# Kernel optimization log

Hardware: AMD Instinct MI355X
Metric: run time of the kernel (lower is better)

The kernel has to match this reference:

```python
import jax, jax.numpy as jnp
import numpy as np

EMBED, HEADS, LEVELS, POINTS = 256, 8, 4, 4
HD = EMBED // HEADS
BS, NQ = 2, 16384
SHAPES = [(128, 128), (64, 64), (32, 32), (16, 16)]  # (H, W) per level
NV = sum(h * w for h, w in SHAPES)
EPS = 1e-5


def layernorm(x, g, b):
    mu = jnp.mean(x, -1, keepdims=True)
    var = jnp.mean((x - mu) ** 2, -1, keepdims=True)
    return (x - mu) / jnp.sqrt(var + EPS) * g + b


def bilinear_sample(vl, loc, H, W):
    # vl: (bs, heads, H*W, hd); loc: (bs, nq, heads, P, 2) normalized [0,1]
    # grid_sample semantics: align_corners=False, zero padding
    x = loc[..., 0] * W - 0.5
    y = loc[..., 1] * H - 0.5
    x0 = jnp.floor(x)
    y0 = jnp.floor(y)
    lx, ly = x - x0, y - y0
    x0 = x0.astype(jnp.int32)
    y0 = y0.astype(jnp.int32)
    gather = jax.vmap(jax.vmap(lambda t, i: t[i]))  # over (bs, heads)
    acc = None
    for dx, dy, w in ((0, 0, (1 - lx) * (1 - ly)), (1, 0, lx * (1 - ly)),
                      (0, 1, (1 - lx) * ly), (1, 1, lx * ly)):
        xi, yi = x0 + dx, y0 + dy
        valid = ((xi >= 0) & (xi < W) & (yi >= 0) & (yi < H)).astype(vl.dtype)
        idx = jnp.clip(yi, 0, H - 1) * W + jnp.clip(xi, 0, W - 1)
        idx = idx.transpose(0, 2, 1, 3)           # (bs, heads, nq, P)
        g = gather(vl, idx)                       # (bs, heads, nq, P, hd)
        wv = (w * valid).transpose(0, 2, 1, 3)[..., None]
        acc = g * wv if acc is None else acc + g * wv
    return acc


def forward(lidar_feat, feat_flatten, ref_2d, spatial_shapes, level_start_index,
            q_pose, W_off, b_off, W_attn, b_attn, W_val, b_val, W_out, b_out,
            ln1_g, ln1_b, ffn_w1, ffn_w2, ln2_g, ln2_b):
    identity = lidar_feat                         # (nq, bs, C)
    q = (lidar_feat + q_pose).transpose(1, 0, 2)  # (bs, nq, C)
    bs, nq, C = q.shape
    v = feat_flatten.transpose(1, 0, 2) @ W_val + b_val
    v = v.reshape(bs, -1, HEADS, HD)
    off = (q @ W_off + b_off).reshape(bs, nq, HEADS, LEVELS, POINTS, 2)
    aw = (q @ W_attn + b_attn).reshape(bs, nq, HEADS, LEVELS * POINTS)
    aw = jax.nn.softmax(aw, -1).reshape(bs, nq, HEADS, LEVELS, POINTS)
    ss = np.asarray(spatial_shapes)               # static level shapes
    lsi = np.asarray(level_start_index)
    norm = jnp.asarray(ss[:, ::-1].copy(), q.dtype)  # (L, 2) [W, H]
    loc = ref_2d[:, :, None, :, None, :] + off / norm[None, None, None, :, None, :]
    out = jnp.zeros((bs, nq, HEADS, HD), q.dtype)
    for l in range(LEVELS):
        H, W = int(ss[l, 0]), int(ss[l, 1])
        s = int(lsi[l])
        vl = v[:, s:s + H * W].transpose(0, 2, 1, 3)   # (bs, heads, HW, hd)
        sampled = bilinear_sample(vl, loc[:, :, :, l], H, W)
        out = out + jnp.einsum('bhqpd,bqhp->bqhd', sampled, aw[:, :, :, l, :])
    out = out.reshape(bs, nq, C) @ W_out + b_out
    out = out.transpose(1, 0, 2) + identity       # residual (dropout=eval noop)
    x = layernorm(out, ln1_g, ln1_b)
    x = layernorm(jnp.maximum(x @ ffn_w1, 0.0) @ ffn_w2 + x, ln2_g, ln2_b)
    return x


def setup_inputs():
    key = jax.random.key(0)
    ks = jax.random.split(key, 16)
    starts = np.cumsum([0] + [h * w for h, w in SHAPES])[:-1]
    d = {
        'lidar_feat': jax.random.normal(ks[0], (NQ, BS, EMBED), jnp.float32),
        'feat_flatten': jax.random.normal(ks[1], (NV, BS, EMBED), jnp.float32),
        'ref_2d': jax.random.uniform(ks[2], (BS, NQ, LEVELS, 2), jnp.float32),
        'spatial_shapes': jnp.array(SHAPES, jnp.int32),
        'level_start_index': jnp.array(starts, jnp.int32),
        'q_pose': jax.random.normal(ks[3], (NQ, BS, EMBED), jnp.float32),
        'W_off': 0.02 * jax.random.normal(ks[4], (EMBED, HEADS * LEVELS * POINTS * 2), jnp.float32),
        'b_off': 2.0 * jax.random.normal(ks[5], (HEADS * LEVELS * POINTS * 2,), jnp.float32),
        'W_attn': 0.02 * jax.random.normal(ks[6], (EMBED, HEADS * LEVELS * POINTS), jnp.float32),
        'b_attn': jnp.zeros((HEADS * LEVELS * POINTS,), jnp.float32),
        'W_val': 0.02 * jax.random.normal(ks[7], (EMBED, EMBED), jnp.float32),
        'b_val': jnp.zeros((EMBED,), jnp.float32),
        'W_out': 0.02 * jax.random.normal(ks[8], (EMBED, EMBED), jnp.float32),
        'b_out': jnp.zeros((EMBED,), jnp.float32),
        'ln1_g': jnp.ones((EMBED,), jnp.float32),
        'ln1_b': jnp.zeros((EMBED,), jnp.float32),
        'ffn_w1': 0.02 * jax.random.normal(ks[9], (EMBED, EMBED), jnp.float32),
        'ffn_w2': 0.02 * jax.random.normal(ks[10], (EMBED, EMBED), jnp.float32),
        'ln2_g': jnp.ones((EMBED,), jnp.float32),
        'ln2_b': jnp.zeros((EMBED,), jnp.float32),
    }
    return d


def reference(lidar_feat, feat_flatten, ref_2d, spatial_shapes, level_start_index,
              q_pose, W_off, b_off, W_attn, b_attn, W_val, b_val, W_out, b_out,
              ln1_g, ln1_b, ffn_w1, ffn_w2, ln2_g, ln2_b):
    return forward(lidar_feat, feat_flatten, ref_2d, spatial_shapes,
                   level_start_index, q_pose, W_off, b_off, W_attn, b_attn,
                   W_val, b_val, W_out, b_out, ln1_g, ln1_b, ffn_w1, ffn_w2,
                   ln2_g, ln2_b)
```

## Files before the change

### kernel.cpp

```cpp
#include <hip/hip_runtime.h>
#include <cstdint>

#define EMBED 256
#define HEADS 8
#define LEVELS 4
#define POINTS 4
#define BS 2
#define NQ 16384
#define NV 21760
#define MQ (BS*NQ)
#define MV (BS*NV)

typedef __attribute__((ext_vector_type(8))) short short8;
typedef __attribute__((ext_vector_type(4))) float f32x4;

__device__ __forceinline__ unsigned short f2bf(float f) {
    unsigned int u = __float_as_uint(f);
    u = (u + 0x7FFFu + ((u >> 16) & 1u)) >> 16;
    return (unsigned short)u;
}
__device__ __forceinline__ float bf2f(unsigned short h) {
    return __uint_as_float(((unsigned int)h) << 16);
}
__device__ __forceinline__ void glds16(const unsigned short* g, unsigned short* l) {
    __builtin_amdgcn_global_load_lds((const __attribute__((address_space(1))) void*)g,
                                     (__attribute__((address_space(3))) void*)l, 16, 0, 0);
}

struct WtArgs {
    const float* src[6];
    unsigned short* dst[6];
    int n[6];
};
__global__ __launch_bounds__(256) void prep_wt(WtArgs a)
{
    const int g = blockIdx.y;
    const int N = a.n[g];
    const int e = blockIdx.x * 256 + threadIdx.x;
    if (e >= 256 * N) return;
    const int k = e / N, n = e - k * N;
    a.dst[g][(size_t)n * 256 + k] = f2bf(a.src[g][e]);
}

template<int NCOLS, int STAGEF32, int LNF, int RELUF>
__global__ __launch_bounds__(512) void gemm_big(
    const unsigned short* __restrict__ A,
    const float* __restrict__ Af, const float* __restrict__ A2f, int inner,
    const unsigned short* __restrict__ Bt,
    const float* __restrict__ bias0, const float* __restrict__ bias1,
    const float* __restrict__ res,
    const float* __restrict__ lng, const float* __restrict__ lnb,
    float* __restrict__ outf, unsigned short* __restrict__ outh)
{
    constexpr int FN = NCOLS / 64;
    __shared__ unsigned short As[128 * 32];
    __shared__ unsigned short Bs[NCOLS * 32];
    __shared__ float2 sdLN[LNF ? 128 : 1][4];

    const int t = threadIdx.x, l = t & 63, w = t >> 6;
    const int wm = w >> 2, wn = w & 3;
    const int frow = l & 15, fgrp = l >> 4;
    const size_t brow = (size_t)blockIdx.x * 128;

    const int fslot = fgrp ^ ((frow & 3) ^ ((frow >> 2) & 3));
    const int srow = l >> 2;
    const int sswz = (l & 3) ^ ((srow & 3) ^ ((srow >> 2) & 3));
    const unsigned short* gB0 = Bt + ((size_t)(w * 16 + srow)) * 256 + sswz * 8;

    const unsigned short* gA = nullptr;
    const float* srcA = nullptr; const float* srcA2 = nullptr;
    int arow_s = 0, aslot_s = 0, aswz_s = 0;
    if constexpr (STAGEF32) {
        arow_s = t >> 2; aslot_s = t & 3;
        const int grow = (int)brow + arow_s;
        const int bidx = grow / inner, nn = grow - bidx * inner;
        srcA = Af + (size_t)(nn * BS + bidx) * 256;
        if (A2f) srcA2 = A2f + (size_t)(nn * BS + bidx) * 256;
        aswz_s = aslot_s ^ ((arow_s & 3) ^ ((arow_s >> 2) & 3));
    } else {
        gA = A + (brow + (size_t)(w * 16 + srow)) * 256 + sswz * 8;
    }

    f32x4 acc[4][FN];
#pragma unroll
    for (int i = 0; i < 4; ++i)
#pragma unroll
        for (int j = 0; j < FN; ++j) acc[i][j] = f32x4{0.f, 0.f, 0.f, 0.f};

    float4 pA0, pA1, pC0, pC1;
    if constexpr (STAGEF32) {
        pA0 = *(const float4*)(srcA + aslot_s * 8);
        pA1 = *(const float4*)(srcA + aslot_s * 8 + 4);
        if (srcA2) { pC0 = *(const float4*)(srcA2 + aslot_s * 8);
                     pC1 = *(const float4*)(srcA2 + aslot_s * 8 + 4); }
    }

    for (int k0 = 0; k0 < 256; k0 += 32) {
        glds16(gB0 + k0,         (unsigned short*)&Bs[w * 512]);
        glds16(gB0 + 32768 + k0, (unsigned short*)&Bs[(w + 8) * 512]);
        if constexpr (NCOLS == 384)
            glds16(gB0 + 65536 + k0, (unsigned short*)&Bs[(w + 16) * 512]);

        if constexpr (STAGEF32) {
            float c[8] = {pA0.x, pA0.y, pA0.z, pA0.w, pA1.x, pA1.y, pA1.z, pA1.w};
            if (srcA2) {
                c[0] += pC0.x; c[1] += pC0.y; c[2] += pC0.z; c[3] += pC0.w;
                c[4] += pC1.x; c[5] += pC1.y; c[6] += pC1.z; c[7] += pC1.w;
            }
            short8 pk;
#pragma unroll
            for (int i = 0; i < 8; ++i) pk[i] = (short)f2bf(c[i]);
            *reinterpret_cast<short8*>(&As[arow_s * 32 + aswz_s * 8]) = pk;
            if (k0 + 32 < 256) {
                pA0 = *(const float4*)(srcA + k0 + 32 + aslot_s * 8);
                pA1 = *(const float4*)(srcA + k0 + 32 + aslot_s * 8 + 4);
                if (srcA2) { pC0 = *(const float4*)(srcA2 + k0 + 32 + aslot_s * 8);
                             pC1 = *(const float4*)(srcA2 + k0 + 32 + aslot_s * 8 + 4); }
            }
        } else {
            glds16(gA + k0, (unsigned short*)&As[w * 512]);
        }
        __syncthreads();

        short8 af[4]; short8 bq[FN];
#pragma unroll
        for (int fm = 0; fm < 4; ++fm)
            af[fm] = *reinterpret_cast<const short8*>(&As[(wm * 64 + fm * 16 + frow) * 32 + fslot * 8]);
#pragma unroll
        for (int fn = 0; fn < FN; ++fn)
            bq[fn] = *reinterpret_cast<const short8*>(&Bs[(wn * (NCOLS / 4) + fn * 16 + frow) * 32 + fslot * 8]);
#pragma unroll
        for (int fm = 0; fm < 4; ++fm)
#pragma unroll
            for (int fn = 0; fn < FN; ++fn)
                acc[fm][fn] = __builtin_amdgcn_mfma_f32_16x16x32_bf16(af[fm], bq[fn], acc[fm][fn], 0, 0, 0);
        __syncthreads();
    }

    int cols[FN]; float bi[FN];
#pragma unroll
    for (int fn = 0; fn < FN; ++fn) {
        const int col = wn * (NCOLS / 4) + fn * 16 + frow;
        cols[fn] = col;
        float b = 0.f;
        if (bias0) {
            if (NCOLS == 384) b = (col < 256) ? bias0[col] : bias1[col - 256];
            else              b = bias0[col];
        }
        bi[fn] = b;
    }
#pragma unroll
    for (int fm = 0; fm < 4; ++fm)
#pragma unroll
        for (int j = 0; j < 4; ++j) {
            const size_t row = brow + wm * 64 + fm * 16 + fgrp * 4 + j;
#pragma unroll
            for (int fn = 0; fn < FN; ++fn) {
                float x = acc[fm][fn][j] + bi[fn];
                if (res)   x += res[row * NCOLS + cols[fn]];
                if (RELUF) x = fmaxf(x, 0.f);
                acc[fm][fn][j] = x;
            }
        }

    if constexpr (LNF) {
#pragma unroll
        for (int fm = 0; fm < 4; ++fm)
#pragma unroll
            for (int j = 0; j < 4; ++j) {
                float s1 = 0.f, s2 = 0.f;
#pragma unroll
                for (int fn = 0; fn < FN; ++fn) { const float x = acc[fm][fn][j]; s1 += x; s2 += x * x; }
#pragma unroll
                for (int o = 1; o < 16; o <<= 1) { s1 += __shfl_xor(s1, o); s2 += __shfl_xor(s2, o); }
                if (frow == 0)
                    sdLN[wm * 64 + fm * 16 + fgrp * 4 + j][wn] = make_float2(s1, s2);
            }
        __syncthreads();
        float gv[FN], bv[FN];
#pragma unroll
        for (int fn = 0; fn < FN; ++fn) { gv[fn] = lng[cols[fn]]; bv[fn] = lnb[cols[fn]]; }
#pragma unroll
        for (int fm = 0; fm < 4; ++fm)
#pragma unroll
            for (int j = 0; j < 4; ++j) {
                const int rl = wm * 64 + fm * 16 + fgrp * 4 + j;
                const float2 p0 = sdLN[rl][0], p1 = sdLN[rl][1], p2 = sdLN[rl][2], p3 = sdLN[rl][3];
                const float s1 = p0.x + p1.x + p2.x + p3.x;
                const float s2 = p0.y + p1.y + p2.y + p3.y;
                const float mu = s1 * (1.f / 256.f);
                const float var = s2 * (1.f / 256.f) - mu * mu;
                const float rstd = rsqrtf(var + 1e-5f);
                const size_t row = brow + rl;
#pragma unroll
                for (int fn = 0; fn < FN; ++fn) {
                    const float y = (acc[fm][fn][j] - mu) * rstd * gv[fn] + bv[fn];
                    if (outf) outf[row * NCOLS + cols[fn]] = y;
                    if (outh) outh[row * NCOLS + cols[fn]] = f2bf(y);
                }
            }
    } else {
#pragma unroll
        for (int fm = 0; fm < 4; ++fm)
#pragma unroll
            for (int j = 0; j < 4; ++j) {
                const size_t row = brow + wm * 64 + fm * 16 + fgrp * 4 + j;
#pragma unroll
                for (int fn = 0; fn < FN; ++fn) {
                    const float x = acc[fm][fn][j];
                    if (outf) outf[row * NCOLS + cols[fn]] = x;
                    if (outh) outh[row * NCOLS + cols[fn]] = f2bf(x);
                }
            }
    }
}

__global__ __launch_bounds__(512) void ffn_fused(
    const unsigned short* __restrict__ X,
    const unsigned short* __restrict__ W1t, const unsigned short* __restrict__ W2t,
    const float* __restrict__ lng, const float* __restrict__ lnb,
    float* __restrict__ outf)
{
    __shared__ unsigned short As[64 * 32];
    __shared__ unsigned short Bs[256 * 32];
    __shared__ unsigned short Hs[64 * 256];
    __shared__ float2 sdLN[64][4];

    const int t = threadIdx.x, l = t & 63, w = t >> 6;
    const int wm = w >> 2, wn = w & 3;
    const int frow = l & 15, fgrp = l >> 4;
    const size_t brow = (size_t)blockIdx.x * 64;

    const int fslot = fgrp ^ ((frow & 3) ^ ((frow >> 2) & 3));
    const int srow = l >> 2;
    const int sswz = (l & 3) ^ ((srow & 3) ^ ((srow >> 2) & 3));

    const unsigned short* gX  = X + (brow + (size_t)((w & 3) * 16 + srow)) * 256 + sswz * 8;
    const unsigned short* gW1 = W1t + ((size_t)(w * 16 + srow)) * 256 + sswz * 8;
    const unsigned short* gW2 = W2t + ((size_t)(w * 16 + srow)) * 256 + sswz * 8;

    f32x4 acc[2][4];

#pragma unroll
    for (int i = 0; i < 2; ++i)
#pragma unroll
        for (int j = 0; j < 4; ++j) acc[i][j] = f32x4{0.f, 0.f, 0.f, 0.f};

    for (int k0 = 0; k0 < 256; k0 += 32) {
        glds16(gW1 + k0,         (unsigned short*)&Bs[w * 512]);
        glds16(gW1 + 32768 + k0, (unsigned short*)&Bs[(w + 8) * 512]);
        if (w < 4) glds16(gX + k0, (unsigned short*)&As[w * 512]);
        __syncthreads();

        short8 af[2], bq[4];
#pragma unroll
        for (int fm = 0; fm < 2; ++fm)
            af[fm] = *reinterpret_cast<const short8*>(&As[(wm * 32 + fm * 16 + frow) * 32 + fslot * 8]);
#pragma unroll
        for (int fn = 0; fn < 4; ++fn)
            bq[fn] = *reinterpret_cast<const short8*>(&Bs[(wn * 64 + fn * 16 + frow) * 32 + fslot * 8]);
#pragma unroll
        for (int fm = 0; fm < 2; ++fm)
#pragma unroll
            for (int fn = 0; fn < 4; ++fn)
                acc[fm][fn] = __builtin_amdgcn_mfma_f32_16x16x32_bf16(af[fm], bq[fn], acc[fm][fn], 0, 0, 0);
        __syncthreads();
    }

#pragma unroll
    for (int fm = 0; fm < 2; ++fm)
#pragma unroll
        for (int fn = 0; fn < 4; ++fn) {
            const int col = wn * 64 + fn * 16 + frow;
#pragma unroll
            for (int j = 0; j < 4; ++j) {
                const int row = wm * 32 + fm * 16 + fgrp * 4 + j;
                const int ss = (col >> 3) ^ (row & 7);
                Hs[row * 256 + ss * 8 + (col & 7)] = f2bf(fmaxf(acc[fm][fn][j], 0.f));
            }
        }
    __syncthreads();

#pragma unroll
    for (int i = 0; i < 2; ++i)
#pragma unroll
        for (int j = 0; j < 4; ++j) acc[i][j] = f32x4{0.f, 0.f, 0.f, 0.f};

    for (int k0 = 0; k0 < 256; k0 += 32) {
        glds16(gW2 + k0,         (unsigned short*)&Bs[w * 512]);
        glds16(gW2 + 32768 + k0, (unsigned short*)&Bs[(w + 8) * 512]);
        __syncthreads();

        short8 af[2], bq[4];
#pragma unroll
        for (int fm = 0; fm < 2; ++fm) {
            const int row = wm * 32 + fm * 16 + frow;
            const int ksg = (k0 >> 3) + fgrp;
            const int ss = ksg ^ (row & 7);
            af[fm] = *reinterpret_cast<const short8*>(&Hs[row * 256 + ss * 8]);
        }
#pragma unroll
        for (int fn = 0; fn < 4; ++fn)
            bq[fn] = *reinterpret_cast<const short8*>(&Bs[(wn * 64 + fn * 16 + frow) * 32 + fslot * 8]);
#pragma unroll
        for (int fm = 0; fm < 2; ++fm)
#pragma unroll
            for (int fn = 0; fn < 4; ++fn)
                acc[fm][fn] = __builtin_amdgcn_mfma_f32_16x16x32_bf16(af[fm], bq[fn], acc[fm][fn], 0, 0, 0);
        __syncthreads();
    }

#pragma unroll
    for (int fm = 0; fm < 2; ++fm)
#pragma unroll
        for (int fn = 0; fn < 4; ++fn) {
            const int col = wn * 64 + fn * 16 + frow;
#pragma unroll
            for (int j = 0; j < 4; ++j) {
                const size_t row = brow + wm * 32 + fm * 16 + fgrp * 4 + j;
                acc[fm][fn][j] += bf2f(X[row * 256 + col]);
            }
        }
#pragma unroll
    for (int fm = 0; fm < 2; ++fm)
#pragma unroll
        for (int j = 0; j < 4; ++j) {
            float s1 = 0.f, s2 = 0.f;
#pragma unroll
            for (int fn = 0; fn < 4; ++fn) { const float x = acc[fm][fn][j]; s1 += x; s2 += x * x; }
#pragma unroll
            for (int o = 1; o < 16; o <<= 1) { s1 += __shfl_xor(s1, o); s2 += __shfl_xor(s2, o); }
            if (frow == 0)
                sdLN[wm * 32 + fm * 16 + fgrp * 4 + j][wn] = make_float2(s1, s2);
        }
    __syncthreads();
#pragma unroll
    for (int fm = 0; fm < 2; ++fm)
#pragma unroll
        for (int j = 0; j < 4; ++j) {
            const int rl = wm * 32 + fm * 16 + fgrp * 4 + j;
            const float2 p0 = sdLN[rl][0], p1 = sdLN[rl][1], p2 = sdLN[rl][2], p3 = sdLN[rl][3];
            const float s1 = p0.x + p1.x + p2.x + p3.x;
            const float s2 = p0.y + p1.y + p2.y + p3.y;
            const float mu = s1 * (1.f / 256.f);
            const float var = s2 * (1.f / 256.f) - mu * mu;
            const float rstd = rsqrtf(var + 1e-5f);
            const size_t row = brow + rl;
#pragma unroll
            for (int fn = 0; fn < 4; ++fn) {
                const int col = wn * 64 + fn * 16 + frow;
                outf[row * 256 + col] = (acc[fm][fn][j] - mu) * rstd * lng[col] + lnb[col];
            }
        }
}

#define LDDESC(dst, base)                         \
    _Pragma("unroll")                             \
    for (int j = 0; j < 16; ++j) dst[j] = dp[(base) + j];
#define LDRAW(dst, dsc)                           \
    _Pragma("unroll")                             \
    for (int j = 0; j < 16; ++j) dst[j] = *(const uint2*)(vd + dsc[j].y);
#define FMA16(dsc, raw)                           \
    _Pragma("unroll")                             \
    for (int j = 0; j < 16; ++j) {                \
        const float wgt = __uint_as_float(dsc[j].x);            \
        a0 += wgt * __uint_as_float(raw[j].x << 16);            \
        a1 += wgt * __uint_as_float(raw[j].x & 0xFFFF0000u);    \
        a2 += wgt * __uint_as_float(raw[j].y << 16);            \
        a3 += wgt * __uint_as_float(raw[j].y & 0xFFFF0000u);    \
    }

__global__ __launch_bounds__(256) void sampler_k(
    const unsigned short* __restrict__ oa,
    const float* __restrict__ ref2d,
    const unsigned short* __restrict__ v,
    unsigned short* __restrict__ outh)
{
    const int q0 = blockIdx.x * 4;
    const int t = threadIdx.x;

    __shared__ float s_off[4][256];
    __shared__ float s_aw[4][128];
    __shared__ float s_ref[4][8];
    __shared__ uint2 s_d[4][8][65];

    {
        const int tq = t >> 6, c = (t & 63) * 4;
        const ushort4 u = *(const ushort4*)(oa + (size_t)(q0 + tq) * 384 + c);
        s_off[tq][c + 0] = bf2f(u.x); s_off[tq][c + 1] = bf2f(u.y);
        s_off[tq][c + 2] = bf2f(u.z); s_off[tq][c + 3] = bf2f(u.w);
    }
    if (t < 128) {
        const int tq = t >> 5, c = (t & 31) * 4;
        const ushort4 u = *(const ushort4*)(oa + (size_t)(q0 + tq) * 384 + 256 + c);
        s_aw[tq][c + 0] = bf2f(u.x); s_aw[tq][c + 1] = bf2f(u.y);
        s_aw[tq][c + 2] = bf2f(u.z); s_aw[tq][c + 3] = bf2f(u.w);
    }
    if (t < 32) {
        const int tq = t >> 3;
        s_ref[tq][t & 7] = ref2d[(size_t)(q0 + tq) * 8 + (t & 7)];
    }
    __syncthreads();

    if (t < 32) {
        const int tq = t >> 3, h = t & 7;
        float* a = s_aw[tq] + h * 16;
        float m = -1e30f;
#pragma unroll
        for (int i = 0; i < 16; ++i) m = fmaxf(m, a[i]);
        float e[16], s = 0.f;
#pragma unroll
        for (int i = 0; i < 16; ++i) { e[i] = __expf(a[i] - m); s += e[i]; }
        const float inv = 1.f / s;
#pragma unroll
        for (int i = 0; i < 16; ++i) a[i] = e[i] * inv;
    }
    __syncthreads();

#pragma unroll
    for (int it = 0; it < 2; ++it) {
        const int item = t + it * 256;
        const int tq = item >> 7, hlp = item & 127;
        const int h = hlp >> 4, lp = hlp & 15, li = lp >> 2;
        const int Wl[4]  = {128, 64, 32, 16};
        const int S0l[4] = {0, 16384, 20480, 21504};
        const int Wi = Wl[li]; const float Wf = (float)Wi;
        const int b = (q0 + tq) >> 14;
        const float x = (s_ref[tq][li * 2 + 0] + s_off[tq][hlp * 2 + 0] / Wf) * Wf - 0.5f;
        const float y = (s_ref[tq][li * 2 + 1] + s_off[tq][hlp * 2 + 1] / Wf) * Wf - 0.5f;
        const float x0f = floorf(x), y0f = floorf(y);
        const float lx = x - x0f, ly = y - y0f;
        const int x0 = (int)x0f, y0 = (int)y0f;
        const float a = s_aw[tq][hlp];
        const float cw[4] = {(1.f - lx) * (1.f - ly) * a, lx * (1.f - ly) * a,
                             (1.f - lx) * ly * a,          lx * ly * a};
        const int base = b * NV + S0l[li];
#pragma unroll
        for (int c = 0; c < 4; ++c) {
            const int xi = x0 + (c & 1), yi = y0 + (c >> 1);
            const bool val = (xi >= 0) & (xi < Wi) & (yi >= 0) & (yi < Wi);
            const int xc = min(max(xi, 0), Wi - 1), yc = min(max(yi, 0), Wi - 1);
            const unsigned int ofs = (unsigned int)(base + yc * Wi + xc) * 256u + h * 32;
            s_d[tq][h][lp * 4 + c] = make_uint2(__float_as_uint(val ? cw[c] : 0.f), ofs);
        }
    }
    __syncthreads();

    const int tq = t >> 6, l = t & 63, h = l >> 3, dq = l & 7;
    const int rb = q0 + tq, b = rb >> 14, qi = rb & (NQ - 1);
    const unsigned short* vd = v + dq * 4;
    const uint2* dp = &s_d[tq][h][0];
    float a0 = 0.f, a1 = 0.f, a2 = 0.f, a3 = 0.f;

    uint2 dA[16], dB[16], rA[16], rB[16];
    LDDESC(dA, 0)
    LDRAW(rA, dA)
    LDDESC(dB, 16)
    LDRAW(rB, dB)
    FMA16(dA, rA)
    LDDESC(dA, 32)
    LDRAW(rA, dA)
    FMA16(dB, rB)
    LDDESC(dB, 48)
    LDRAW(rB, dB)
    FMA16(dA, rA)
    FMA16(dB, rB)

    ushort4 o; o.x = f2bf(a0); o.y = f2bf(a1); o.z = f2bf(a2); o.w = f2bf(a3);
    *(ushort4*)(outh + (size_t)(qi * BS + b) * 256 + h * 32 + dq * 4) = o;
}

extern "C" void kernel_launch(void* const* d_in, const int* in_sizes, int n_in,
                              void* d_out, int out_size, void* d_ws, size_t ws_size,
                              hipStream_t stream)
{
    const float* lidar  = (const float*)d_in[0];
    const float* feat   = (const float*)d_in[1];
    const float* ref2d  = (const float*)d_in[2];
    const float* q_pose = (const float*)d_in[5];
    const float* W_off  = (const float*)d_in[6];
    const float* b_off  = (const float*)d_in[7];
    const float* W_attn = (const float*)d_in[8];
    const float* b_attn = (const float*)d_in[9];
    const float* W_val  = (const float*)d_in[10];
    const float* b_val  = (const float*)d_in[11];
    const float* W_out  = (const float*)d_in[12];
    const float* b_out  = (const float*)d_in[13];
    const float* ln1_g  = (const float*)d_in[14];
    const float* ln1_b  = (const float*)d_in[15];
    const float* ffn_w1 = (const float*)d_in[16];
    const float* ffn_w2 = (const float*)d_in[17];
    const float* ln2_g  = (const float*)d_in[18];
    const float* ln2_b  = (const float*)d_in[19];

    float* out = (float*)d_out;
    char*  ws  = (char*)d_ws;

    unsigned short* vb   = (unsigned short*)(ws + 0);
    unsigned short* oa   = (unsigned short*)(ws + 22282240);
    unsigned short* smp  = (unsigned short*)(ws + 47448064);
    unsigned short* xln  = (unsigned short*)(ws + 64225280);
    unsigned short* wt   = (unsigned short*)(ws + 81002496);
    unsigned short* wt_val = wt;
    unsigned short* wt_oa  = wt + 65536;
    unsigned short* wt_out = wt + 163840;
    unsigned short* wt_f1  = wt + 229376;
    unsigned short* wt_f2  = wt + 294912;

    WtArgs wa;
    wa.src[0] = W_val;  wa.dst[0] = wt_val;          wa.n[0] = 256;
    wa.src[1] = W_off;  wa.dst[1] = wt_oa;           wa.n[1] = 256;
    wa.src[2] = W_attn; wa.dst[2] = wt_oa + 65536;   wa.n[2] = 128;
    wa.src[3] = W_out;  wa.dst[3] = wt_out;          wa.n[3] = 256;
    wa.src[4] = ffn_w1; wa.dst[4] = wt_f1;           wa.n[4] = 256;
    wa.src[5] = ffn_w2; wa.dst[5] = wt_f2;           wa.n[5] = 256;
    prep_wt<<<dim3(384, 6), dim3(256), 0, stream>>>(wa);

    gemm_big<256, 1, 0, 0><<<dim3(MV / 128), dim3(512), 0, stream>>>(
        nullptr, feat, nullptr, NV, wt_val, b_val, nullptr,
        nullptr, nullptr, nullptr, nullptr, vb);

    gemm_big<384, 1, 0, 0><<<dim3(MQ / 128), dim3(512), 0, stream>>>(
        nullptr, lidar, q_pose, NQ, wt_oa, b_off, b_attn,
        nullptr, nullptr, nullptr, nullptr, oa);

    sampler_k<<<dim3(MQ / 4), dim3(256), 0, stream>>>(oa, ref2d, vb, smp);

    gemm_big<256, 0, 1, 0><<<dim3(MQ / 128), dim3(512), 0, stream>>>(
        smp, nullptr, nullptr, 0, wt_out, b_out, nullptr,
        lidar, ln1_g, ln1_b, nullptr, xln);

    ffn_fused<<<dim3(MQ / 64), dim3(512), 0, stream>>>(
        xln, wt_f1, wt_f2, ln2_g, ln2_b, out);
}
```

Before: 204.5 us.

## Fuse value/offset GEMMs, sort queries spatially, and fuse out-proj with FFN

```diff
diff --git a/kernel.cpp b/kernel.cpp
--- a/kernel.cpp
+++ b/kernel.cpp
@@ -10,6 +10,9 @@
 #define NV 21760
 #define MQ (BS*NQ)
 #define MV (BS*NV)
+#define VAL_BLK 340
+#define OA_BLK  256
+#define BKT_BLK 64
 
 typedef __attribute__((ext_vector_type(8))) short short8;
 typedef __attribute__((ext_vector_type(4))) float f32x4;
@@ -32,54 +35,43 @@
     unsigned short* dst[6];
     int n[6];
 };
-__global__ __launch_bounds__(256) void prep_wt(WtArgs a)
-{
+__global__ __launch_bounds__(256) void prep_wt(WtArgs a, int* __restrict__ hist)
+{
+    const int t = threadIdx.x;
+    if (blockIdx.x == 0 && blockIdx.y == 0) { hist[t] = 0; hist[t + 256] = 0; }
     const int g = blockIdx.y;
     const int N = a.n[g];
-    const int e = blockIdx.x * 256 + threadIdx.x;
+    const int e = blockIdx.x * 256 + t;
     if (e >= 256 * N) return;
     const int k = e / N, n = e - k * N;
     a.dst[g][(size_t)n * 256 + k] = f2bf(a.src[g][e]);
 }
 
-template<int NCOLS, int STAGEF32, int LNF, int RELUF>
-__global__ __launch_bounds__(512) void gemm_big(
-    const unsigned short* __restrict__ A,
+template<int NCOLS>
+__device__ __forceinline__ void gemm_core(
+    unsigned short* As, unsigned short* Bs, int bx,
     const float* __restrict__ Af, const float* __restrict__ A2f, int inner,
     const unsigned short* __restrict__ Bt,
     const float* __restrict__ bias0, const float* __restrict__ bias1,
-    const float* __restrict__ res,
-    const float* __restrict__ lng, const float* __restrict__ lnb,
-    float* __restrict__ outf, unsigned short* __restrict__ outh)
+    unsigned short* __restrict__ outh)
 {
     constexpr int FN = NCOLS / 64;
-    __shared__ unsigned short As[128 * 32];
-    __shared__ unsigned short Bs[NCOLS * 32];
-    __shared__ float2 sdLN[LNF ? 128 : 1][4];
-
     const int t = threadIdx.x, l = t & 63, w = t >> 6;
     const int wm = w >> 2, wn = w & 3;
     const int frow = l & 15, fgrp = l >> 4;
-    const size_t brow = (size_t)blockIdx.x * 128;
+    const size_t brow = (size_t)bx * 128;
 
     const int fslot = fgrp ^ ((frow & 3) ^ ((frow >> 2) & 3));
     const int srow = l >> 2;
     const int sswz = (l & 3) ^ ((srow & 3) ^ ((srow >> 2) & 3));
     const unsigned short* gB0 = Bt + ((size_t)(w * 16 + srow)) * 256 + sswz * 8;
 
-    const unsigned short* gA = nullptr;
-    const float* srcA = nullptr; const float* srcA2 = nullptr;
-    int arow_s = 0, aslot_s = 0, aswz_s = 0;
-    if constexpr (STAGEF32) {
-        arow_s = t >> 2; aslot_s = t & 3;
-        const int grow = (int)brow + arow_s;
-        const int bidx = grow / inner, nn = grow - bidx * inner;
-        srcA = Af + (size_t)(nn * BS + bidx) * 256;
-        if (A2f) srcA2 = A2f + (size_t)(nn * BS + bidx) * 256;
-        aswz_s = aslot_s ^ ((arow_s & 3) ^ ((arow_s >> 2) & 3));
-    } else {
-        gA = A + (brow + (size_t)(w * 16 + srow)) * 256 + sswz * 8;
-    }
+    const int arow_s = t >> 2, aslot_s = t & 3;
+    const int grow = (int)brow + arow_s;
+    const int bidx = grow / inner, nn = grow - bidx * inner;
+    const float* srcA = Af + (size_t)(nn * BS + bidx) * 256;
+    const float* srcA2 = A2f ? A2f + (size_t)(nn * BS + bidx) * 256 : nullptr;
+    const int aswz_s = aslot_s ^ ((arow_s & 3) ^ ((arow_s >> 2) & 3));
 
     f32x4 acc[4][FN];
 #pragma unroll
@@ -87,38 +79,32 @@
 #pragma unroll
         for (int j = 0; j < FN; ++j) acc[i][j] = f32x4{0.f, 0.f, 0.f, 0.f};
 
-    float4 pA0, pA1, pC0, pC1;
-    if constexpr (STAGEF32) {
-        pA0 = *(const float4*)(srcA + aslot_s * 8);
-        pA1 = *(const float4*)(srcA + aslot_s * 8 + 4);
-        if (srcA2) { pC0 = *(const float4*)(srcA2 + aslot_s * 8);
-                     pC1 = *(const float4*)(srcA2 + aslot_s * 8 + 4); }
-    }
+    float4 pA0 = *(const float4*)(srcA + aslot_s * 8);
+    float4 pA1 = *(const float4*)(srcA + aslot_s * 8 + 4);
+    float4 pC0, pC1;
+    if (srcA2) { pC0 = *(const float4*)(srcA2 + aslot_s * 8);
+                 pC1 = *(const float4*)(srcA2 + aslot_s * 8 + 4); }
 
     for (int k0 = 0; k0 < 256; k0 += 32) {
-        glds16(gB0 + k0,         (unsigned short*)&Bs[w * 512]);
-        glds16(gB0 + 32768 + k0, (unsigned short*)&Bs[(w + 8) * 512]);
+        glds16(gB0 + k0,         &Bs[w * 512]);
+        glds16(gB0 + 32768 + k0, &Bs[(w + 8) * 512]);
         if constexpr (NCOLS == 384)
-            glds16(gB0 + 65536 + k0, (unsigned short*)&Bs[(w + 16) * 512]);
-
-        if constexpr (STAGEF32) {
-            float c[8] = {pA0.x, pA0.y, pA0.z, pA0.w, pA1.x, pA1.y, pA1.z, pA1.w};
-            if (srcA2) {
-                c[0] += pC0.x; c[1] += pC0.y; c[2] += pC0.z; c[3] += pC0.w;
-                c[4] += pC1.x; c[5] += pC1.y; c[6] += pC1.z; c[7] += pC1.w;
-            }
-            short8 pk;
-#pragma unroll
-            for (int i = 0; i < 8; ++i) pk[i] = (short)f2bf(c[i]);
-            *reinterpret_cast<short8*>(&As[arow_s * 32 + aswz_s * 8]) = pk;
-            if (k0 + 32 < 256) {
-                pA0 = *(const float4*)(srcA + k0 + 32 + aslot_s * 8);
-                pA1 = *(const float4*)(srcA + k0 + 32 + aslot_s * 8 + 4);
-                if (srcA2) { pC0 = *(const float4*)(srcA2 + k0 + 32 + aslot_s * 8);
-                             pC1 = *(const float4*)(srcA2 + k0 + 32 + aslot_s * 8 + 4); }
-            }
-        } else {
-            glds16(gA + k0, (unsigned short*)&As[w * 512]);
+            glds16(gB0 + 65536 + k0, &Bs[(w + 16) * 512]);
+
+        float c[8] = {pA0.x, pA0.y, pA0.z, pA0.w, pA1.x, pA1.y, pA1.z, pA1.w};
+        if (srcA2) {
+            c[0] += pC0.x; c[1] += pC0.y; c[2] += pC0.z; c[3] += pC0.w;
+            c[4] += pC1.x; c[5] += pC1.y; c[6] += pC1.z; c[7] += pC1.w;
+        }
+        short8 pk;
+#pragma unroll
+        for (int i = 0; i < 8; ++i) pk[i] = (short)f2bf(c[i]);
+        *reinterpret_cast<short8*>(&As[arow_s * 32 + aswz_s * 8]) = pk;
+        if (k0 + 32 < 256) {
+            pA0 = *(const float4*)(srcA + k0 + 32 + aslot_s * 8);
+            pA1 = *(const float4*)(srcA + k0 + 32 + aslot_s * 8 + 4);
+            if (srcA2) { pC0 = *(const float4*)(srcA2 + k0 + 32 + aslot_s * 8);
+                         pC1 = *(const float4*)(srcA2 + k0 + 32 + aslot_s * 8 + 4); }
         }
         __syncthreads();
 
@@ -137,93 +123,166 @@
         __syncthreads();
     }
 
-    int cols[FN]; float bi[FN];
 #pragma unroll
     for (int fn = 0; fn < FN; ++fn) {
         const int col = wn * (NCOLS / 4) + fn * 16 + frow;
-        cols[fn] = col;
         float b = 0.f;
-        if (bias0) {
-            if (NCOLS == 384) b = (col < 256) ? bias0[col] : bias1[col - 256];
-            else              b = bias0[col];
-        }
-        bi[fn] = b;
-    }
-#pragma unroll
-    for (int fm = 0; fm < 4; ++fm)
-#pragma unroll
-        for (int j = 0; j < 4; ++j) {
-            const size_t row = brow + wm * 64 + fm * 16 + fgrp * 4 + j;
-#pragma unroll
-            for (int fn = 0; fn < FN; ++fn) {
-                float x = acc[fm][fn][j] + bi[fn];
-                if (res)   x += res[row * NCOLS + cols[fn]];
-                if (RELUF) x = fmaxf(x, 0.f);
-                acc[fm][fn][j] = x;
-            }
-        }
-
-    if constexpr (LNF) {
-#pragma unroll
-        for (int fm = 0; fm < 4; ++fm)
-#pragma unroll
-            for (int j = 0; j < 4; ++j) {
-                float s1 = 0.f, s2 = 0.f;
-#pragma unroll
-                for (int fn = 0; fn < FN; ++fn) { const float x = acc[fm][fn][j]; s1 += x; s2 += x * x; }
-#pragma unroll
-                for (int o = 1; o < 16; o <<= 1) { s1 += __shfl_xor(s1, o); s2 += __shfl_xor(s2, o); }
-                if (frow == 0)
-                    sdLN[wm * 64 + fm * 16 + fgrp * 4 + j][wn] = make_float2(s1, s2);
-            }
-        __syncthreads();
-        float gv[FN], bv[FN];
-#pragma unroll
-        for (int fn = 0; fn < FN; ++fn) { gv[fn] = lng[cols[fn]]; bv[fn] = lnb[cols[fn]]; }
-#pragma unroll
-        for (int fm = 0; fm < 4; ++fm)
-#pragma unroll
-            for (int j = 0; j < 4; ++j) {
-                const int rl = wm * 64 + fm * 16 + fgrp * 4 + j;
-                const float2 p0 = sdLN[rl][0], p1 = sdLN[rl][1], p2 = sdLN[rl][2], p3 = sdLN[rl][3];
-                const float s1 = p0.x + p1.x + p2.x + p3.x;
-                const float s2 = p0.y + p1.y + p2.y + p3.y;
-                const float mu = s1 * (1.f / 256.f);
-                const float var = s2 * (1.f / 256.f) - mu * mu;
-                const float rstd = rsqrtf(var + 1e-5f);
-                const size_t row = brow + rl;
-#pragma unroll
-                for (int fn = 0; fn < FN; ++fn) {
-                    const float y = (acc[fm][fn][j] - mu) * rstd * gv[fn] + bv[fn];
-                    if (outf) outf[row * NCOLS + cols[fn]] = y;
-                    if (outh) outh[row * NCOLS + cols[fn]] = f2bf(y);
-                }
-            }
-    } else {
+        if (NCOLS == 384) b = (col < 256) ? bias0[col] : bias1[col - 256];
+        else              b = bias0[col];
 #pragma unroll
         for (int fm = 0; fm < 4; ++fm)
 #pragma unroll
             for (int j = 0; j < 4; ++j) {
                 const size_t row = brow + wm * 64 + fm * 16 + fgrp * 4 + j;
-#pragma unroll
-                for (int fn = 0; fn < FN; ++fn) {
-                    const float x = acc[fm][fn][j];
-                    if (outf) outf[row * NCOLS + cols[fn]] = x;
-                    if (outh) outh[row * NCOLS + cols[fn]] = f2bf(x);
-                }
+                outh[row * NCOLS + col] = f2bf(acc[fm][fn][j] + b);
             }
     }
 }
 
-__global__ __launch_bounds__(512) void ffn_fused(
-    const unsigned short* __restrict__ X,
-    const unsigned short* __restrict__ W1t, const unsigned short* __restrict__ W2t,
-    const float* __restrict__ lng, const float* __restrict__ lnb,
+__global__ __launch_bounds__(512) void valoa_k(
+    const float* __restrict__ feat, const float* __restrict__ lidar,
+    const float* __restrict__ q_pose, const float* __restrict__ ref2d,
+    const unsigned short* __restrict__ wt_val, const unsigned short* __restrict__ wt_oa,
+    const float* __restrict__ b_val, const float* __restrict__ b_off,
+    const float* __restrict__ b_attn,
+    unsigned short* __restrict__ vb, unsigned short* __restrict__ oa,
+    int* __restrict__ bkt, int* __restrict__ hist)
+{
+    __shared__ unsigned short As[128 * 32];
+    __shared__ unsigned short Bs[384 * 32];
+    const int bx = blockIdx.x;
+    if (bx < VAL_BLK) {
+        gemm_core<256>(As, Bs, bx, feat, nullptr, NV, wt_val, b_val, nullptr, vb);
+    } else if (bx < VAL_BLK + OA_BLK) {
+        gemm_core<384>(As, Bs, bx - VAL_BLK, lidar, q_pose, NQ, wt_oa, b_off, b_attn, oa);
+    } else {
+        const int rb = (bx - VAL_BLK - OA_BLK) * 512 + threadIdx.x;
+        const float x = ref2d[(size_t)rb * 8 + 0];
+        const float y = ref2d[(size_t)rb * 8 + 1];
+        const int qx = min(15, max(0, (int)(x * 16.f)));
+        const int qy = min(15, max(0, (int)(y * 16.f)));
+        const int bv = (rb >> 14) * 256 + qy * 16 + qx;
+        bkt[rb] = bv;
+        atomicAdd(&hist[bv], 1);
+    }
+}
+
+__global__ __launch_bounds__(512) void scan_scatter_k(
+    const int* __restrict__ hist, const int* __restrict__ bkt, int* __restrict__ perm)
+{
+    __shared__ int s[512];
+    __shared__ int cur[512];
+    const int t = threadIdx.x;
+    const int v = hist[t];
+    s[t] = v;
+    __syncthreads();
+    int acc = v;
+#pragma unroll
+    for (int o = 1; o < 512; o <<= 1) {
+        const int add = (t >= o) ? s[t - o] : 0;
+        __syncthreads();
+        acc += add;
+        s[t] = acc;
+        __syncthreads();
+    }
+    cur[t] = acc - v;
+    __syncthreads();
+#pragma unroll 4
+    for (int i = 0; i < 64; ++i) {
+        const int rb = i * 512 + t;
+        const int pos = atomicAdd(&cur[bkt[rb]], 1);
+        perm[pos] = rb;
+    }
+}
+
+__global__ __launch_bounds__(256) void sampler_k(
+    const unsigned short* __restrict__ oa,
+    const float* __restrict__ ref2d,
+    const unsigned short* __restrict__ v,
+    const int* __restrict__ perm,
+    unsigned short* __restrict__ outh)
+{
+    const int bid = blockIdx.x;
+    const int sbid = (bid & 7) * (MQ / 4 / 8) + (bid >> 3);
+    const int q0 = sbid * 4;
+    const int t = threadIdx.x;
+
+    __shared__ uint2 s_d[4][8][4][17];
+
+#pragma unroll
+    for (int it = 0; it < 2; ++it) {
+        const int item = t + it * 256;
+        const int tq = item >> 7, hlp = item & 127;
+        const int h = hlp >> 4, lp = hlp & 15, li = lp >> 2;
+        const int rb = perm[q0 + tq];
+        const int b = rb >> 14;
+
+        const float2 refv = *(const float2*)(ref2d + (size_t)rb * 8 + li * 2);
+        const ushort2 offu = *(const ushort2*)(oa + (size_t)rb * 384 + hlp * 2);
+        const float ax = bf2f(oa[(size_t)rb * 384 + 256 + hlp]);
+
+        float m = ax;
+#pragma unroll
+        for (int o = 1; o < 16; o <<= 1) m = fmaxf(m, __shfl_xor(m, o));
+        const float e = __expf(ax - m);
+        float sden = e;
+#pragma unroll
+        for (int o = 1; o < 16; o <<= 1) sden += __shfl_xor(sden, o);
+        const float a = e / sden;
+
+        const int Wl[4]  = {128, 64, 32, 16};
+        const int S0l[4] = {0, 16384, 20480, 21504};
+        const int Wi = Wl[li]; const float Wf = (float)Wi;
+        const float x = (refv.x + bf2f(offu.x) / Wf) * Wf - 0.5f;
+        const float y = (refv.y + bf2f(offu.y) / Wf) * Wf - 0.5f;
+        const float x0f = floorf(x), y0f = floorf(y);
+        const float lx = x - x0f, ly = y - y0f;
+        const int x0 = (int)x0f, y0 = (int)y0f;
+        const float cw[4] = {(1.f - lx) * (1.f - ly) * a, lx * (1.f - ly) * a,
+                             (1.f - lx) * ly * a,          lx * ly * a};
+        const int base = b * NV + S0l[li];
+#pragma unroll
+        for (int c = 0; c < 4; ++c) {
+            const int xi = x0 + (c & 1), yi = y0 + (c >> 1);
+            const bool val = (xi >= 0) & (xi < Wi) & (yi >= 0) & (yi < Wi);
+            const int xc = min(max(xi, 0), Wi - 1), yc = min(max(yi, 0), Wi - 1);
+            const unsigned int ofs = (unsigned int)(base + yc * Wi + xc) * 256u + h * 32;
+            s_d[tq][h][c][lp] = make_uint2(__float_as_uint(val ? cw[c] : 0.f), ofs);
+        }
+    }
+    __syncthreads();
+
+    const int tq = t >> 6, l = t & 63, h = l >> 3, dq = l & 7;
+    const int rb = perm[q0 + tq], b = rb >> 14, qi = rb & (NQ - 1);
+    const unsigned short* vd = v + dq * 4;
+    float a0 = 0.f, a1 = 0.f, a2 = 0.f, a3 = 0.f;
+#pragma unroll
+    for (int c = 0; c < 4; ++c) {
+#pragma unroll
+        for (int i = 0; i < 16; ++i) {
+            const uint2 dd = s_d[tq][h][c][i];
+            const uint2 raw = *(const uint2*)(vd + dd.y);
+            const float wgt = __uint_as_float(dd.x);
+            a0 += wgt * __uint_as_float(raw.x << 16);
+            a1 += wgt * __uint_as_float(raw.x & 0xFFFF0000u);
+            a2 += wgt * __uint_as_float(raw.y << 16);
+            a3 += wgt * __uint_as_float(raw.y & 0xFFFF0000u);
+        }
+    }
+    ushort4 o; o.x = f2bf(a0); o.y = f2bf(a1); o.z = f2bf(a2); o.w = f2bf(a3);
+    *(ushort4*)(outh + (size_t)(qi * BS + b) * 256 + h * 32 + dq * 4) = o;
+}
+
+__global__ __launch_bounds__(512) void mega_k(
+    const unsigned short* __restrict__ smp, const float* __restrict__ lidar,
+    const unsigned short* __restrict__ Wo, const unsigned short* __restrict__ W1,
+    const unsigned short* __restrict__ W2, const float* __restrict__ b_out,
+    const float* __restrict__ ln1g, const float* __restrict__ ln1b,
+    const float* __restrict__ ln2g, const float* __restrict__ ln2b,
     float* __restrict__ outf)
 {
-    __shared__ unsigned short As[64 * 32];
+    __shared__ unsigned short XH[64 * 256];
     __shared__ unsigned short Bs[256 * 32];
-    __shared__ unsigned short Hs[64 * 256];
     __shared__ float2 sdLN[64][4];
 
     const int t = threadIdx.x, l = t & 63, w = t >> 6;
@@ -235,11 +294,13 @@
     const int srow = l >> 2;
     const int sswz = (l & 3) ^ ((srow & 3) ^ ((srow >> 2) & 3));
 
-    const unsigned short* gX  = X + (brow + (size_t)((w & 3) * 16 + srow)) * 256 + sswz * 8;
-    const unsigned short* gW1 = W1t + ((size_t)(w * 16 + srow)) * 256 + sswz * 8;
-    const unsigned short* gW2 = W2t + ((size_t)(w * 16 + srow)) * 256 + sswz * 8;
+    const unsigned short* gA  = smp + (brow + (size_t)((w & 3) * 16 + srow)) * 256 + sswz * 8;
+    const unsigned short* gWo = Wo + ((size_t)(w * 16 + srow)) * 256 + sswz * 8;
+    const unsigned short* gW1 = W1 + ((size_t)(w * 16 + srow)) * 256 + sswz * 8;
+    const unsigned short* gW2 = W2 + ((size_t)(w * 16 + srow)) * 256 + sswz * 8;
 
     f32x4 acc[2][4];
+    f32x4 xres[2][4];
 
 #pragma unroll
     for (int i = 0; i < 2; ++i)
@@ -247,15 +308,14 @@
         for (int j = 0; j < 4; ++j) acc[i][j] = f32x4{0.f, 0.f, 0.f, 0.f};
 
     for (int k0 = 0; k0 < 256; k0 += 32) {
-        glds16(gW1 + k0,         (unsigned short*)&Bs[w * 512]);
-        glds16(gW1 + 32768 + k0, (unsigned short*)&Bs[(w + 8) * 512]);
-        if (w < 4) glds16(gX + k0, (unsigned short*)&As[w * 512]);
-        __syncthreads();
-
+        glds16(gWo + k0,         &Bs[w * 512]);
+        glds16(gWo + 32768 + k0, &Bs[(w + 8) * 512]);
+        if (w < 4) glds16(gA + k0, &XH[w * 512]);
+        __syncthreads();
         short8 af[2], bq[4];
 #pragma unroll
         for (int fm = 0; fm < 2; ++fm)
-            af[fm] = *reinterpret_cast<const short8*>(&As[(wm * 32 + fm * 16 + frow) * 32 + fslot * 8]);
+            af[fm] = *reinterpret_cast<const short8*>(&XH[(wm * 32 + fm * 16 + frow) * 32 + fslot * 8]);
 #pragma unroll
         for (int fn = 0; fn < 4; ++fn)
             bq[fn] = *reinterpret_cast<const short8*>(&Bs[(wn * 64 + fn * 16 + frow) * 32 + fslot * 8]);
@@ -272,13 +332,45 @@
 #pragma unroll
         for (int fn = 0; fn < 4; ++fn) {
             const int col = wn * 64 + fn * 16 + frow;
+            const float bv = b_out[col];
 #pragma unroll
             for (int j = 0; j < 4; ++j) {
-                const int row = wm * 32 + fm * 16 + fgrp * 4 + j;
-                const int ss = (col >> 3) ^ (row & 7);
-                Hs[row * 256 + ss * 8 + (col & 7)] = f2bf(fmaxf(acc[fm][fn][j], 0.f));
+                const size_t row = brow + wm * 32 + fm * 16 + fgrp * 4 + j;
+                acc[fm][fn][j] += bv + lidar[row * 256 + col];
             }
         }
+#pragma unroll
+    for (int fm = 0; fm < 2; ++fm)
+#pragma unroll
+        for (int j = 0; j < 4; ++j) {
+            float s1 = 0.f, s2 = 0.f;
+#pragma unroll
+            for (int fn = 0; fn < 4; ++fn) { const float x = acc[fm][fn][j]; s1 += x; s2 += x * x; }
+#pragma unroll
+            for (int o = 1; o < 16; o <<= 1) { s1 += __shfl_xor(s1, o); s2 += __shfl_xor(s2, o); }
+            if (frow == 0) sdLN[wm * 32 + fm * 16 + fgrp * 4 + j][wn] = make_float2(s1, s2);
+        }
+    __syncthreads();
+#pragma unroll
+    for (int fm = 0; fm < 2; ++fm)
+#pragma unroll
+        for (int j = 0; j < 4; ++j) {
+            const int rl = wm * 32 + fm * 16 + fgrp * 4 + j;
+            const float2 p0 = sdLN[rl][0], p1 = sdLN[rl][1], p2 = sdLN[rl][2], p3 = sdLN[rl][3];
+            const float s1 = p0.x + p1.x + p2.x + p3.x;
+            const float s2 = p0.y + p1.y + p2.y + p3.y;
+            const float mu = s1 * (1.f / 256.f);
+            const float var = s2 * (1.f / 256.f) - mu * mu;
+            const float rstd = rsqrtf(var + 1e-5f);
+#pragma unroll
+            for (int fn = 0; fn < 4; ++fn) {
+                const int col = wn * 64 + fn * 16 + frow;
+                const float y = (acc[fm][fn][j] - mu) * rstd * ln1g[col] + ln1b[col];
+                xres[fm][fn][j] = y;
+                const int ss = (col >> 3) ^ (rl & 7);
+                XH[rl * 256 + ss * 8 + (col & 7)] = f2bf(y);
+            }
+        }
     __syncthreads();
 
 #pragma unroll
@@ -287,17 +379,15 @@
         for (int j = 0; j < 4; ++j) acc[i][j] = f32x4{0.f, 0.f, 0.f, 0.f};
 
     for (int k0 = 0; k0 < 256; k0 += 32) {
-        glds16(gW2 + k0,         (unsigned short*)&Bs[w * 512]);
-        glds16(gW2 + 32768 + k0, (unsigned short*)&Bs[(w + 8) * 512]);
-        __syncthreads();
-
+        glds16(gW1 + k0,         &Bs[w * 512]);
+        glds16(gW1 + 32768 + k0, &Bs[(w + 8) * 512]);
+        __syncthreads();
         short8 af[2], bq[4];
 #pragma unroll
         for (int fm = 0; fm < 2; ++fm) {
             const int row = wm * 32 + fm * 16 + frow;
-            const int ksg = (k0 >> 3) + fgrp;
-            const int ss = ksg ^ (row & 7);
-            af[fm] = *reinterpret_cast<const short8*>(&Hs[row * 256 + ss * 8]);
+            const int ss = ((k0 >> 3) + fgrp) ^ (row & 7);
+            af[fm] = *reinterpret_cast<const short8*>(&XH[row * 256 + ss * 8]);
         }
 #pragma unroll
         for (int fn = 0; fn < 4; ++fn)
@@ -317,10 +407,46 @@
             const int col = wn * 64 + fn * 16 + frow;
 #pragma unroll
             for (int j = 0; j < 4; ++j) {
-                const size_t row = brow + wm * 32 + fm * 16 + fgrp * 4 + j;
-                acc[fm][fn][j] += bf2f(X[row * 256 + col]);
+                const int rl = wm * 32 + fm * 16 + fgrp * 4 + j;
+                const int ss = (col >> 3) ^ (rl & 7);
+                XH[rl * 256 + ss * 8 + (col & 7)] = f2bf(fmaxf(acc[fm][fn][j], 0.f));
             }
         }
+    __syncthreads();
+
+#pragma unroll
+    for (int i = 0; i < 2; ++i)
+#pragma unroll
+        for (int j = 0; j < 4; ++j) acc[i][j] = f32x4{0.f, 0.f, 0.f, 0.f};
+
+    for (int k0 = 0; k0 < 256; k0 += 32) {
+        glds16(gW2 + k0,         &Bs[w * 512]);
+        glds16(gW2 + 32768 + k0, &Bs[(w + 8) * 512]);
+        __syncthreads();
+        short8 af[2], bq[4];
+#pragma unroll
+        for (int fm = 0; fm < 2; ++fm) {
+            const int row = wm * 32 + fm * 16 + frow;
+            const int ss = ((k0 >> 3) + fgrp) ^ (row & 7);
+            af[fm] = *reinterpret_cast<const short8*>(&XH[row * 256 + ss * 8]);
+        }
+#pragma unroll
+        for (int fn = 0; fn < 4; ++fn)
+            bq[fn] = *reinterpret_cast<const short8*>(&Bs[(wn * 64 + fn * 16 + frow) * 32 + fslot * 8]);
+#pragma unroll
+        for (int fm = 0; fm < 2; ++fm)
+#pragma unroll
+            for (int fn = 0; fn < 4; ++fn)
+                acc[fm][fn] = __builtin_amdgcn_mfma_f32_16x16x32_bf16(af[fm], bq[fn], acc[fm][fn], 0, 0, 0);
+        __syncthreads();
+    }
+
+#pragma unroll
+    for (int fm = 0; fm < 2; ++fm)
+#pragma unroll
+        for (int fn = 0; fn < 4; ++fn)
+#pragma unroll
+            for (int j = 0; j < 4; ++j) acc[fm][fn][j] += xres[fm][fn][j];
 #pragma unroll
     for (int fm = 0; fm < 2; ++fm)
 #pragma unroll
@@ -330,8 +456,7 @@
             for (int fn = 0; fn < 4; ++fn) { const float x = acc[fm][fn][j]; s1 += x; s2 += x * x; }
 #pragma unroll
             for (int o = 1; o < 16; o <<= 1) { s1 += __shfl_xor(s1, o); s2 += __shfl_xor(s2, o); }
-            if (frow == 0)
-                sdLN[wm * 32 + fm * 16 + fgrp * 4 + j][wn] = make_float2(s1, s2);
+            if (frow == 0) sdLN[wm * 32 + fm * 16 + fgrp * 4 + j][wn] = make_float2(s1, s2);
         }
     __syncthreads();
 #pragma unroll
@@ -349,125 +474,9 @@
 #pragma unroll
             for (int fn = 0; fn < 4; ++fn) {
                 const int col = wn * 64 + fn * 16 + frow;
-                outf[row * 256 + col] = (acc[fm][fn][j] - mu) * rstd * lng[col] + lnb[col];
+                outf[row * 256 + col] = (acc[fm][fn][j] - mu) * rstd * ln2g[col] + ln2b[col];
             }
         }
-}
-
-#define LDDESC(dst, base)                         \
-    _Pragma("unroll")                             \
-    for (int j = 0; j < 16; ++j) dst[j] = dp[(base) + j];
-#define LDRAW(dst, dsc)                           \
-    _Pragma("unroll")                             \
-    for (int j = 0; j < 16; ++j) dst[j] = *(const uint2*)(vd + dsc[j].y);
-#define FMA16(dsc, raw)                           \
-    _Pragma("unroll")                             \
-    for (int j = 0; j < 16; ++j) {                \
-        const float wgt = __uint_as_float(dsc[j].x);            \
-        a0 += wgt * __uint_as_float(raw[j].x << 16);            \
-        a1 += wgt * __uint_as_float(raw[j].x & 0xFFFF0000u);    \
-        a2 += wgt * __uint_as_float(raw[j].y << 16);            \
-        a3 += wgt * __uint_as_float(raw[j].y & 0xFFFF0000u);    \
-    }
-
-__global__ __launch_bounds__(256) void sampler_k(
-    const unsigned short* __restrict__ oa,
-    const float* __restrict__ ref2d,
-    const unsigned short* __restrict__ v,
-    unsigned short* __restrict__ outh)
-{
-    const int q0 = blockIdx.x * 4;
-    const int t = threadIdx.x;
-
-    __shared__ float s_off[4][256];
-    __shared__ float s_aw[4][128];
-    __shared__ float s_ref[4][8];
-    __shared__ uint2 s_d[4][8][65];
-
-    {
-        const int tq = t >> 6, c = (t & 63) * 4;
-        const ushort4 u = *(const ushort4*)(oa + (size_t)(q0 + tq) * 384 + c);
-        s_off[tq][c + 0] = bf2f(u.x); s_off[tq][c + 1] = bf2f(u.y);
-        s_off[tq][c + 2] = bf2f(u.z); s_off[tq][c + 3] = bf2f(u.w);
-    }
-    if (t < 128) {
-        const int tq = t >> 5, c = (t & 31) * 4;
-        const ushort4 u = *(const ushort4*)(oa + (size_t)(q0 + tq) * 384 + 256 + c);
-        s_aw[tq][c + 0] = bf2f(u.x); s_aw[tq][c + 1] = bf2f(u.y);
-        s_aw[tq][c + 2] = bf2f(u.z); s_aw[tq][c + 3] = bf2f(u.w);
-    }
-    if (t < 32) {
-        const int tq = t >> 3;
-        s_ref[tq][t & 7] = ref2d[(size_t)(q0 + tq) * 8 + (t & 7)];
-    }
-    __syncthreads();
-
-    if (t < 32) {
-        const int tq = t >> 3, h = t & 7;
-        float* a = s_aw[tq] + h * 16;
-        float m = -1e30f;
-#pragma unroll
-        for (int i = 0; i < 16; ++i) m = fmaxf(m, a[i]);
-        float e[16], s = 0.f;
-#pragma unroll
-        for (int i = 0; i < 16; ++i) { e[i] = __expf(a[i] - m); s += e[i]; }
-        const float inv = 1.f / s;
-#pragma unroll
-        for (int i = 0; i < 16; ++i) a[i] = e[i] * inv;
-    }
-    __syncthreads();
-
-#pragma unroll
-    for (int it = 0; it < 2; ++it) {
-        const int item = t + it * 256;
-        const int tq = item >> 7, hlp = item & 127;
-        const int h = hlp >> 4, lp = hlp & 15, li = lp >> 2;
-        const int Wl[4]  = {128, 64, 32, 16};
-        const int S0l[4] = {0, 16384, 20480, 21504};
-        const int Wi = Wl[li]; const float Wf = (float)Wi;
-        const int b = (q0 + tq) >> 14;
-        const float x = (s_ref[tq][li * 2 + 0] + s_off[tq][hlp * 2 + 0] / Wf) * Wf - 0.5f;
-        const float y = (s_ref[tq][li * 2 + 1] + s_off[tq][hlp * 2 + 1] / Wf) * Wf - 0.5f;
-        const float x0f = floorf(x), y0f = floorf(y);
-        const float lx = x - x0f, ly = y - y0f;
-        const int x0 = (int)x0f, y0 = (int)y0f;
-        const float a = s_aw[tq][hlp];
-        const float cw[4] = {(1.f - lx) * (1.f - ly) * a, lx * (1.f - ly) * a,
-                             (1.f - lx) * ly * a,          lx * ly * a};
-        const int base = b * NV + S0l[li];
-#pragma unroll
-        for (int c = 0; c < 4; ++c) {
-            const int xi = x0 + (c & 1), yi = y0 + (c >> 1);
-            const bool val = (xi >= 0) & (xi < Wi) & (yi >= 0) & (yi < Wi);
-            const int xc = min(max(xi, 0), Wi - 1), yc = min(max(yi, 0), Wi - 1);
-            const unsigned int ofs = (unsigned int)(base + yc * Wi + xc) * 256u + h * 32;
-            s_d[tq][h][lp * 4 + c] = make_uint2(__float_as_uint(val ? cw[c] : 0.f), ofs);
-        }
-    }
-    __syncthreads();
-
-    const int tq = t >> 6, l = t & 63, h = l >> 3, dq = l & 7;
-    const int rb = q0 + tq, b = rb >> 14, qi = rb & (NQ - 1);
-    const unsigned short* vd = v + dq * 4;
-    const uint2* dp = &s_d[tq][h][0];
-    float a0 = 0.f, a1 = 0.f, a2 = 0.f, a3 = 0.f;
-
-    uint2 dA[16], dB[16], rA[16], rB[16];
-    LDDESC(dA, 0)
-    LDRAW(rA, dA)
-    LDDESC(dB, 16)
-    LDRAW(rB, dB)
-    FMA16(dA, rA)
-    LDDESC(dA, 32)
-    LDRAW(rA, dA)
-    FMA16(dB, rB)
-    LDDESC(dB, 48)
-    LDRAW(rB, dB)
-    FMA16(dA, rA)
-    FMA16(dB, rB)
-
-    ushort4 o; o.x = f2bf(a0); o.y = f2bf(a1); o.z = f2bf(a2); o.w = f2bf(a3);
-    *(ushort4*)(outh + (size_t)(qi * BS + b) * 256 + h * 32 + dq * 4) = o;
 }
 
 extern "C" void kernel_launch(void* const* d_in, const int* in_sizes, int n_in,
@@ -499,8 +508,10 @@
     unsigned short* vb   = (unsigned short*)(ws + 0);
     unsigned short* oa   = (unsigned short*)(ws + 22282240);
     unsigned short* smp  = (unsigned short*)(ws + 47448064);
-    unsigned short* xln  = (unsigned short*)(ws + 64225280);
-    unsigned short* wt   = (unsigned short*)(ws + 81002496);
+    unsigned short* wt   = (unsigned short*)(ws + 64225280);
+    int* perm = (int*)(ws + 64946176);
+    int* bkt  = (int*)(ws + 65077248);
+    int* hist = (int*)(ws + 65208320);
     unsigned short* wt_val = wt;
     unsigned short* wt_oa  = wt + 65536;
     unsigned short* wt_out = wt + 163840;
@@ -514,22 +525,18 @@
     wa.src[3] = W_out;  wa.dst[3] = wt_out;          wa.n[3] = 256;
     wa.src[4] = ffn_w1; wa.dst[4] = wt_f1;           wa.n[4] = 256;
     wa.src[5] = ffn_w2; wa.dst[5] = wt_f2;           wa.n[5] = 256;
-    prep_wt<<<dim3(384, 6), dim3(256), 0, stream>>>(wa);
-
-    gemm_big<256, 1, 0, 0><<<dim3(MV / 128), dim3(512), 0, stream>>>(
-        nullptr, feat, nullptr, NV, wt_val, b_val, nullptr,
-        nullptr, nullptr, nullptr, nullptr, vb);
-
-    gemm_big<384, 1, 0, 0><<<dim3(MQ / 128), dim3(512), 0, stream>>>(
-        nullptr, lidar, q_pose, NQ, wt_oa, b_off, b_attn,
-        nullptr, nullptr, nullptr, nullptr, oa);
-
-    sampler_k<<<dim3(MQ / 4), dim3(256), 0, stream>>>(oa, ref2d, vb, smp);
-
-    gemm_big<256, 0, 1, 0><<<dim3(MQ / 128), dim3(512), 0, stream>>>(
-        smp, nullptr, nullptr, 0, wt_out, b_out, nullptr,
-        lidar, ln1_g, ln1_b, nullptr, xln);
-
-    ffn_fused<<<dim3(MQ / 64), dim3(512), 0, stream>>>(
-        xln, wt_f1, wt_f2, ln2_g, ln2_b, out);
-}
+
+    prep_wt<<<dim3(384, 6), dim3(256), 0, stream>>>(wa, hist);
+
+    valoa_k<<<dim3(VAL_BLK + OA_BLK + BKT_BLK), dim3(512), 0, stream>>>(
+        feat, lidar, q_pose, ref2d, wt_val, wt_oa, b_val, b_off, b_attn,
+        vb, oa, bkt, hist);
+
+    scan_scatter_k<<<dim3(1), dim3(512), 0, stream>>>(hist, bkt, perm);
+
+    sampler_k<<<dim3(MQ / 4), dim3(256), 0, stream>>>(oa, ref2d, vb, perm, smp);
+
+    mega_k<<<dim3(MQ / 64), dim3(512), 0, stream>>>(
+        smp, lidar, wt_out, wt_f1, wt_f2, b_out,
+        ln1_g, ln1_b, ln2_g, ln2_b, out);
+}
```

Result: slower. 212.2 us (+3.8%).
